# Performance work log

Hardware: AMD Instinct MI355X
Metric: run time of the kernel (lower is better)

Reference implementation:

```python
import jax, jax.numpy as jnp
import numpy as np

B, C, F = 4, 512, 2048
N, H = 8, 64  # header_size, header_channels
ALPHA = 1.0 / np.sqrt(H)


def setup_inputs() -> dict:
    key = jax.random.key(0)
    ks = jax.random.split(key, 6)
    return {
        "from_tensor": jax.random.normal(ks[0], (B, C, F), jnp.float32),
        "to_tensor": jax.random.normal(ks[1], (B, C, F), jnp.float32),
        "mask": jnp.ones((B, F, F), jnp.float32),
        "Wq": jax.random.normal(ks[2], (N * H, C), jnp.float32) * 0.02,
        "bq": jnp.zeros((N * H,), jnp.float32),
        "Wk": jax.random.normal(ks[3], (N * H, C), jnp.float32) * 0.02,
        "bk": jnp.zeros((N * H,), jnp.float32),
        "Wv": jax.random.normal(ks[4], (N * H, C), jnp.float32) * 0.02,
        "bv": jnp.zeros((N * H,), jnp.float32),
    }


def reference(from_tensor, to_tensor, mask, Wq, bq, Wk, bk, Wv, bv):
    b, _, f = from_tensor.shape
    t = to_tensor.shape[2]
    # Dense over channel dim: [B,C,F] -> [B,N*H,F], then split heads
    q = (jnp.einsum("oc,bcf->bof", Wq, from_tensor) + bq[None, :, None]).reshape(b, N, H, f)
    k = (jnp.einsum("oc,bct->bot", Wk, to_tensor) + bk[None, :, None]).reshape(b, N, H, t)
    v = (jnp.einsum("oc,bct->bot", Wv, to_tensor) + bv[None, :, None]).reshape(b, N, H, t)
    # score: q^T @ k -> [B,N,F,T]
    score = jnp.einsum("bnhf,bnht->bnft", q, k) * ALPHA
    score = score + (1.0 - mask[:, None]) * -100000.0
    probs = jax.nn.softmax(score, axis=-1)  # dropout=0 (inference)
    # context: probs @ v^T -> [B,N,F,H], transpose -> [B,N,H,F]
    ctx = jnp.einsum("bnft,bnht->bnhf", probs, v)
    return ctx.reshape(b, N * H, f)
```

## Files before the change

### kernel.cpp

```cpp
#include <hip/hip_runtime.h>

typedef __bf16 bf16x8 __attribute__((ext_vector_type(8)));
typedef float f32x4 __attribute__((ext_vector_type(4)));
typedef float f32x16 __attribute__((ext_vector_type(16)));
typedef unsigned short u16;
typedef u16 u16x8 __attribute__((ext_vector_type(8)));
typedef unsigned int u32;
typedef u32 u32x4 __attribute__((ext_vector_type(4)));
typedef unsigned long long u64;

#define DEVFN static __device__ __forceinline__

DEVFN u16 f2bf(float x) {
  u32 u = __builtin_bit_cast(u32, x);
  u32 r = u + 0x7FFFu + ((u >> 16) & 1u);
  return (u16)(r >> 16);
}

DEVFN float myexp2(float x) {
#if __has_builtin(__builtin_amdgcn_exp2f)
  return __builtin_amdgcn_exp2f(x);
#else
  return exp2f(x);
#endif
}

DEVFN u32 cvt_pk_bf16(float lo, float hi) {
  u32 r;
  asm("v_cvt_pk_bf16_f32 %0, %1, %2" : "=v"(r) : "v"(lo), "v"(hi));
  return r;
}

__global__ __launch_bounds__(512, 6) void proj_kernel(
    const float* __restrict__ from_t, const float* __restrict__ to_t,
    const float* __restrict__ Wq, const float* __restrict__ bq,
    const float* __restrict__ Wk, const float* __restrict__ bk,
    const float* __restrict__ Wv, const float* __restrict__ bv,
    u16* __restrict__ qt, u16* __restrict__ kt, u16* __restrict__ vt) {
  const int d     = blockIdx.x;
  const int xcd   = d & 7;
  const int b     = xcd >> 1;
  const int fh    = xcd & 1;
  const int local = d >> 3;
  const int mat   = local >> 5;
  const int o0    = ((local >> 3) & 3) * 128;
  const int f0    = (fh * 8 + (local & 7)) * 128;

  const float* X    = (mat == 0) ? from_t : to_t;
  const float* W    = (mat == 0) ? Wq : (mat == 1 ? Wk : Wv);
  const float* bias = (mat == 0) ? bq : (mat == 1 ? bk : bv);
  const bool isT = (mat < 2);

  __shared__ u16 Xs[128][64];
  __shared__ u16 Ws[128][64];

  const int tid  = threadIdx.x;
  const int lane = tid & 63;
  const int w    = tid >> 6;

  f32x4 acc[2][4];
#pragma unroll
  for (int i = 0; i < 2; ++i)
#pragma unroll
    for (int j = 0; j < 4; ++j)
#pragma unroll
      for (int r = 0; r < 4; ++r) acc[i][j][r] = 0.f;

  const int arow0 = (w & 3) * 32;
  const int brow0 = (w >> 2) * 64;

  for (int c0 = 0; c0 < 512; c0 += 64) {
    __syncthreads();
#pragma unroll
    for (int i = 0; i < 2; ++i) {
      const int task = tid + 512 * i;
      const int f = task & 127, cg = task >> 7;
      const float* xp = X + ((size_t)b * 512 + c0 + cg * 8) * 2048 + f0 + f;
      float xv[8];
#pragma unroll
      for (int j = 0; j < 8; ++j) xv[j] = xp[(size_t)j * 2048];
      u32x4 pk;
#pragma unroll
      for (int j = 0; j < 4; ++j) pk[j] = cvt_pk_bf16(xv[2 * j], xv[2 * j + 1]);
      *(u32x4*)&Xs[f][(cg ^ (f & 7)) * 8] = pk;
    }
#pragma unroll
    for (int i = 0; i < 2; ++i) {
      const int task = tid + 512 * i;
      const int o = task & 127, cg = task >> 7;
      const float* wp = W + (size_t)(o0 + o) * 512 + c0 + cg * 8;
      const float4 w0 = *(const float4*)(wp);
      const float4 w1 = *(const float4*)(wp + 4);
      u32x4 pk;
      pk[0] = cvt_pk_bf16(w0.x, w0.y);
      pk[1] = cvt_pk_bf16(w0.z, w0.w);
      pk[2] = cvt_pk_bf16(w1.x, w1.y);
      pk[3] = cvt_pk_bf16(w1.z, w1.w);
      *(u32x4*)&Ws[o][(cg ^ (o & 7)) * 8] = pk;
    }
    __syncthreads();

#pragma unroll
    for (int kk = 0; kk < 2; ++kk) {
      const int cb8 = kk * 4;
      bf16x8 afr[2], bfr[4];
#pragma unroll
      for (int mi = 0; mi < 2; ++mi) {
        const int row = arow0 + mi * 16 + (lane & 15);
        const int ch  = (cb8 + (lane >> 4)) ^ (row & 7);
        afr[mi] = *(const bf16x8*)&(isT ? Xs : Ws)[row][ch * 8];
      }
#pragma unroll
      for (int ni = 0; ni < 4; ++ni) {
        const int row = brow0 + ni * 16 + (lane & 15);
        const int ch  = (cb8 + (lane >> 4)) ^ (row & 7);
        bfr[ni] = *(const bf16x8*)&(isT ? Ws : Xs)[row][ch * 8];
      }
#pragma unroll
      for (int mi = 0; mi < 2; ++mi)
#pragma unroll
        for (int ni = 0; ni < 4; ++ni)
          acc[mi][ni] = __builtin_amdgcn_mfma_f32_16x16x32_bf16(
              afr[mi], bfr[ni], acc[mi][ni], 0, 0, 0);
    }
  }

  const float qscale = 0.18033688011112042f;
#pragma unroll
  for (int mi = 0; mi < 2; ++mi)
#pragma unroll
    for (int ni = 0; ni < 4; ++ni)
#pragma unroll
      for (int r = 0; r < 4; ++r) {
        const int rA = arow0 + mi * 16 + (lane >> 4) * 4 + r;
        const int cB = brow0 + ni * 16 + (lane & 15);
        int f, o;
        if (isT) { f = f0 + rA; o = o0 + cB; }
        else     { o = o0 + rA; f = f0 + cB; }
        float val = acc[mi][ni][r] + bias[o];
        if (mat == 0) val *= qscale;
        const u16 hv = f2bf(val);
        if (isT) {
          u16* dst = (mat == 0) ? qt : kt;
          dst[(((size_t)b * 8 + (o >> 6)) * 2048 + f) * 64 + (o & 63)] = hv;
        } else {
          vt[((size_t)b * 512 + o) * 2048 + f] = hv;
        }
      }
}

__global__ __launch_bounds__(256, 4) void maskflag_kernel(
    const float* __restrict__ mask, u32* __restrict__ fmask) {
  const int d    = blockIdx.x;
  const int b    = d >> 9;
  const int ft   = (d >> 5) & 15;
  const int tile = d & 31;
  const int t    = threadIdx.x;

  const float* base =
      mask + ((size_t)b * 2048 + ft * 128) * 2048 + tile * 64;
  bool ok = true;
#pragma unroll
  for (int i = 0; i < 8; ++i) {
    const int row = (t >> 4) * 8 + i;
    const float4 v = *(const float4*)(base + (size_t)row * 2048 + (t & 15) * 4);
    ok = ok && (v.x == 1.0f) && (v.y == 1.0f) && (v.z == 1.0f) && (v.w == 1.0f);
  }
  const u64 bal = __ballot(ok);
  __shared__ u32 wok[4];
  if ((t & 63) == 0) wok[t >> 6] = (bal == ~0ull) ? 1u : 0u;
  __syncthreads();
  if (t == 0) {
    const u32 allok = wok[0] & wok[1] & wok[2] & wok[3];
    if (allok) atomicOr(&fmask[b * 16 + ft], 1u << tile);
  }
}

#define SB __builtin_amdgcn_sched_barrier(0)

#define STAGE(BB, T0)                                                          \
  do {                                                                         \
    __builtin_amdgcn_global_load_lds(                                          \
        (const __attribute__((address_space(1))) void*)(ksrc1 + (size_t)(T0) * 64), \
        (__attribute__((address_space(3))) void*)&Ks[BB][w * 16][0], 16, 0, 0);\
    __builtin_amdgcn_global_load_lds(                                          \
        (const __attribute__((address_space(1))) void*)(ksrc2 + (size_t)(T0) * 64), \
        (__attribute__((address_space(3))) void*)&Ks[BB][w * 16 + 8][0], 16, 0, 0); \
    __builtin_amdgcn_global_load_lds(                                          \
        (const __attribute__((address_space(1))) void*)(vsrc1 + (T0)),         \
        (__attribute__((address_space(3))) void*)&Vs[BB][w * 16][0], 16, 0, 0);\
    __builtin_amdgcn_global_load_lds(                                          \
        (const __attribute__((address_space(1))) void*)(vsrc2 + (T0)),         \
        (__attribute__((address_space(3))) void*)&Vs[BB][w * 16 + 8][0], 16, 0, 0); \
  } while (0)

#define LDK(BUF)                                                               \
  do {                                                                         \
    _Pragma("unroll")                                                          \
    for (int kf_ = 0; kf_ < 4; ++kf_)                                          \
      _Pragma("unroll")                                                        \
      for (int mi_ = 0; mi_ < 2; ++mi_) {                                      \
        const int row_ = mi_ * 32 + fl;                                        \
        kreg[mi_][kf_] =                                                       \
            *(const bf16x8*)&Ks[BUF][row_][((kf_ * 2 + g) ^ (row_ & 7)) * 8];  \
      }                                                                        \
  } while (0)

#define LDV(BUF)                                                               \
  do {                                                                         \
    _Pragma("unroll")                                                          \
    for (int tf_ = 0; tf_ < 4; ++tf_)                                          \
      _Pragma("unroll")                                                        \
      for (int mh_ = 0; mh_ < 2; ++mh_) {                                      \
        const int row_ = mh_ * 32 + fl;                                        \
        vreg[mh_][tf_] =                                                       \
            *(const bf16x8*)&Vs[BUF][row_][((tf_ * 2 + g) ^ (row_ & 7)) * 8];  \
      }                                                                        \
  } while (0)

#define QKMM(SN)                                                               \
  do {                                                                         \
    _Pragma("unroll")                                                          \
    for (int m_ = 0; m_ < 2; ++m_)                                             \
      _Pragma("unroll")                                                        \
      for (int r_ = 0; r_ < 16; ++r_) SN[m_][r_] = 0.f;                        \
    _Pragma("unroll")                                                          \
    for (int kf_ = 0; kf_ < 4; ++kf_)                                          \
      _Pragma("unroll")                                                        \
      for (int mi_ = 0; mi_ < 2; ++mi_)                                        \
        SN[mi_] = __builtin_amdgcn_mfma_f32_32x32x16_bf16(kreg[mi_][kf_],      \
                                                          qf[kf_], SN[mi_],    \
                                                          0, 0, 0);            \
  } while (0)

#define ROUND(RB, SC, SN, T0)                                                  \
  {                                                                            \
    asm volatile("s_waitcnt vmcnt(0)" ::: "memory");                           \
    SB;                                                                        \
    __builtin_amdgcn_s_barrier();                                              \
    SB;                                                                        \
    LDV(RB);                                                                   \
    LDK((RB + 1) & 3);                                                         \
    SB;                                                                        \
    STAGE((RB + 2) & 3, ((T0) + 128) & 2047);                                  \
    SB;                                                                        \
    QKMM(SN);           \
                  \
    if (!((fmask >> ((T0) >> 6)) & 1u)) {                                      \
      float4 mk[8];                                                            \
      _Pragma("unroll")                                                        \
      for (int i_ = 0; i_ < 8; ++i_)                                           \
        mk[i_] = *(const float4*)(mrow + (T0) + (i_ >> 2) * 32 +               \
                                  (i_ & 3) * 8 + g * 4);                       \
      _Pragma("unroll")                                                        \
      for (int mi = 0; mi < 2; ++mi)                                           \
        _Pragma("unroll")                                                      \
        for (int q = 0; q < 4; ++q) {                                          \
          const float4 mv = mk[mi * 4 + q];                                    \
          SC[mi][q * 4 + 0] = fmaf(mv.x - 1.f, 144269.50408889634f, SC[mi][q * 4 + 0]); \
          SC[mi][q * 4 + 1] = fmaf(mv.y - 1.f, 144269.50408889634f, SC[mi][q * 4 + 1]); \
          SC[mi][q * 4 + 2] = fmaf(mv.z - 1.f, 144269.50408889634f, SC[mi][q * 4 + 2]); \
          SC[mi][q * 4 + 3] = fmaf(mv.w - 1.f, 144269.50408889634f, SC[mi][q * 4 + 3]); \
        }                                                                      \
    }                                                                          \
    float ps0 = 0.f, ps1 = 0.f, ps2 = 0.f, ps3 = 0.f;                          \
    _Pragma("unroll")                                                          \
    for (int mi = 0; mi < 2; ++mi)                                             \
      _Pragma("unroll")                                                        \
      for (int r = 0; r < 16; r += 4) {                                        \
        SC[mi][r + 0] = myexp2(SC[mi][r + 0]); ps0 += SC[mi][r + 0];           \
        SC[mi][r + 1] = myexp2(SC[mi][r + 1]); ps1 += SC[mi][r + 1];           \
        SC[mi][r + 2] = myexp2(SC[mi][r + 2]); ps2 += SC[mi][r + 2];           \
        SC[mi][r + 3] = myexp2(SC[mi][r + 3]); ps3 += SC[mi][r + 3];           \
      }                                                                        \
    {                                                                          \
      float ps = (ps0 + ps1) + (ps2 + ps3);                                    \
      ps += __shfl_xor(ps, 32, 64);                                            \
      L += ps;                                                                 \
    }                                                                          \
        \
    u32 dwv[2][4][2];                                                          \
    _Pragma("unroll")                                                          \
    for (int mi = 0; mi < 2; ++mi)                                             \
      _Pragma("unroll")                                                        \
      for (int q = 0; q < 4; ++q) {                                            \
        dwv[mi][q][0] = cvt_pk_bf16(SC[mi][q * 4 + 0], SC[mi][q * 4 + 1]);     \
        dwv[mi][q][1] = cvt_pk_bf16(SC[mi][q * 4 + 2], SC[mi][q * 4 + 3]);     \
      }                                                                        \
    _Pragma("unroll")                                                          \
    for (int tf = 0; tf < 4; ++tf) {                                           \
      const int m_ = tf >> 1, bq2 = tf & 1;                                    \
      u32 A0 = dwv[m_][bq2 * 2][0], A1 = dwv[m_][bq2 * 2][1];                  \
      u32 C0 = dwv[m_][bq2 * 2 + 1][0], C1 = dwv[m_][bq2 * 2 + 1][1];          \
      asm("v_permlane32_swap_b32 %0, %1" : "+v"(A0), "+v"(C0));                \
      asm("v_permlane32_swap_b32 %0, %1" : "+v"(A1), "+v"(C1));                \
      u32x4 pw; pw[0] = A0; pw[1] = A1; pw[2] = C0; pw[3] = C1;                \
      const bf16x8 pfr = __builtin_bit_cast(bf16x8, pw);                       \
      _Pragma("unroll")                                                        \
      for (int mih = 0; mih < 2; ++mih)                                        \
        ctx[mih] = __builtin_amdgcn_mfma_f32_32x32x16_bf16(vreg[mih][tf], pfr, \
                                                           ctx[mih], 0, 0, 0); \
    }                                                                          \
  }

__global__ __launch_bounds__(256, 2) void attn_kernel(
    const float* __restrict__ mask, const u32* __restrict__ fmaskbuf,
    const u16* __restrict__ qt, const u16* __restrict__ kt,
    const u16* __restrict__ vt, float* __restrict__ out) {
  const int d     = blockIdx.x;
  const int xcd   = d & 7;
  const int b     = xcd >> 1;
  const int fthi  = xcd & 1;
  const int local = d >> 3;
  const int n     = local & 7;
  const int ft    = fthi * 8 + (local >> 3);

  const int tid  = threadIdx.x;
  const int lane = tid & 63;
  const int w    = tid >> 6;
  const int g    = lane >> 5;
  const int fl   = lane & 31;
  const int f    = ft * 128 + w * 32 + fl;

  const u16* qtb = qt + ((size_t)b * 8 + n) * 2048 * 64;
  const u16* ktb = kt + ((size_t)b * 8 + n) * 2048 * 64;
  const u16* vb  = vt + ((size_t)b * 512 + n * 64) * 2048;
  const float* mrow = mask + ((size_t)b * 2048 + f) * 2048;
  const u32 fmask = fmaskbuf ? fmaskbuf[b * 16 + ft] : 0u;

  __shared__ u16 Ks[4][64][64];
  __shared__ u16 Vs[4][64][64];

  bf16x8 qf[4];
#pragma unroll
  for (int kf = 0; kf < 4; ++kf)
    qf[kf] = *(const bf16x8*)(qtb + (size_t)f * 64 + kf * 16 + g * 8);

  f32x16 ctx[2];
#pragma unroll
  for (int m = 0; m < 2; ++m)
#pragma unroll
    for (int r = 0; r < 16; ++r) ctx[m][r] = 0.f;
  float L = 0.f;

  const int sr1 = w * 16 + (lane >> 3), sr2 = sr1 + 8;
  const int sc1 = (lane & 7) ^ (sr1 & 7), sc2 = (lane & 7) ^ (sr2 & 7);
  const u16* ksrc1 = ktb + (size_t)sr1 * 64 + sc1 * 8;
  const u16* ksrc2 = ktb + (size_t)sr2 * 64 + sc2 * 8;
  const u16* vsrc1 = vb + (size_t)sr1 * 2048 + sc1 * 8;
  const u16* vsrc2 = vb + (size_t)sr2 * 2048 + sc2 * 8;

  bf16x8 kreg[2][4], vreg[2][4];
  f32x16 sA[2], sB[2];

  STAGE(0, 0);
  STAGE(1, 64);
  SB;
  asm volatile("s_waitcnt vmcnt(0)" ::: "memory");
  SB;
  __builtin_amdgcn_s_barrier();
  SB;
  LDK(0);
  QKMM(sA);

  for (int t0 = 0; t0 < 2048; t0 += 256) {
    ROUND(0, sA, sB, t0);
    ROUND(1, sB, sA, t0 + 64);
    ROUND(2, sA, sB, t0 + 128);
    ROUND(3, sB, sA, t0 + 192);
  }

  const float Linv = 1.0f / L;
#pragma unroll
  for (int mih = 0; mih < 2; ++mih)
#pragma unroll
    for (int r = 0; r < 16; ++r) {
      const int h = mih * 32 + (r & 3) + 8 * (r >> 2) + 4 * g;
      out[((size_t)b * 512 + n * 64 + h) * 2048 + f] = ctx[mih][r] * Linv;
    }
}

extern "C" void kernel_launch(void* const* d_in, const int* in_sizes, int n_in,
                              void* d_out, int out_size, void* d_ws, size_t ws_size,
                              hipStream_t stream) {
  const float* from_t = (const float*)d_in[0];
  const float* to_t   = (const float*)d_in[1];
  const float* mask   = (const float*)d_in[2];
  const float* Wq     = (const float*)d_in[3];
  const float* bq     = (const float*)d_in[4];
  const float* Wk     = (const float*)d_in[5];
  const float* bk     = (const float*)d_in[6];
  const float* Wv     = (const float*)d_in[7];
  const float* bv     = (const float*)d_in[8];
  float* out = (float*)d_out;

  u16* qt = (u16*)d_ws;
  u16* kt = qt + (size_t)4 * 8 * 2048 * 64;
  u16* vt = kt + (size_t)4 * 8 * 2048 * 64;
  const size_t base = (size_t)24 * 1024 * 1024;
  u32* fl = (ws_size >= base + 256) ? (u32*)((char*)d_ws + base) : nullptr;

  proj_kernel<<<dim3(768), 512, 0, stream>>>(from_t, to_t, Wq, bq, Wk, bk,
                                             Wv, bv, qt, kt, vt);
  if (fl) {
    hipMemsetAsync(fl, 0, 64 * sizeof(u32), stream);
    maskflag_kernel<<<dim3(2048), 256, 0, stream>>>(mask, fl);
  }
  attn_kernel<<<dim3(512), 256, 0, stream>>>(mask, fl, qt, kt, vt, out);
}
```

Measured before the change: 112.9 us.

## Fuse mask-flag scan into projection kernel as extra interleaved blocks

Merges the separate mask-scanning kernel into the projection kernel by adding 1024 extra blocks that scan mask tiles alongside the 768 projection blocks, saving one kernel launch. The bandwidth-bound mask reads can then overlap with the compute-bound projection GEMM. Mask loads now use nontemporal hints and each block covers a 128x128 tile, setting two flag bits. This adds grid index arithmetic, and because the projection and scan blocks share one kernel, the scan blocks run under the projection kernel's 512-thread launch configuration.

```diff
diff --git a/kernel.cpp b/kernel.cpp
--- a/kernel.cpp
+++ b/kernel.cpp
@@ -3,6 +3,7 @@
 typedef __bf16 bf16x8 __attribute__((ext_vector_type(8)));
 typedef float f32x4 __attribute__((ext_vector_type(4)));
 typedef float f32x16 __attribute__((ext_vector_type(16)));
+typedef float fvec4 __attribute__((ext_vector_type(4)));
 typedef unsigned short u16;
 typedef u16 u16x8 __attribute__((ext_vector_type(8)));
 typedef unsigned int u32;
@@ -31,17 +32,64 @@
   return r;
 }
 
-__global__ __launch_bounds__(512, 6) void proj_kernel(
+__global__ __launch_bounds__(512, 6) void projflag_kernel(
     const float* __restrict__ from_t, const float* __restrict__ to_t,
+    const float* __restrict__ mask,
     const float* __restrict__ Wq, const float* __restrict__ bq,
     const float* __restrict__ Wk, const float* __restrict__ bk,
     const float* __restrict__ Wv, const float* __restrict__ bv,
-    u16* __restrict__ qt, u16* __restrict__ kt, u16* __restrict__ vt) {
-  const int d     = blockIdx.x;
-  const int xcd   = d & 7;
+    u16* __restrict__ qt, u16* __restrict__ kt, u16* __restrict__ vt,
+    u32* __restrict__ fmask) {
+  __shared__ u16 Xs[128][64];
+  __shared__ u16 Ws[128][64];
+
+  const int bid = blockIdx.x;
+  const int xcd = bid & 7;
+  const int li  = bid >> 3;
+  const int grp = li / 7, rem = li % 7;
+  const int tid = threadIdx.x;
+
+  if (rem >= 3) {
+    if (!fmask) return;
+    const int idx = xcd * 128 + grp * 4 + (rem - 3);
+    const int b   = idx >> 8;
+    const int ft  = (idx >> 4) & 15;
+    const int tp  = idx & 15;
+    const int r   = tid >> 2;
+    const int q   = tid & 3;
+    const float* base = mask + ((size_t)(b * 2048 + ft * 128 + r)) * 2048 +
+                        tp * 128 + q * 32;
+    bool ok = true;
+#pragma unroll
+    for (int j = 0; j < 8; ++j) {
+      const fvec4 v = __builtin_nontemporal_load((const fvec4*)(base) + j);
+      ok = ok && (v[0] == 1.0f) && (v[1] == 1.0f) && (v[2] == 1.0f) &&
+           (v[3] == 1.0f);
+    }
+    const bool lo = (q < 2);
+    const u64 blo = __ballot(ok || !lo);
+    const u64 bhi = __ballot(ok || lo);
+    u32* wok = (u32*)&Xs[0][0];
+    const int w8 = tid >> 6;
+    if ((tid & 63) == 0) {
+      wok[w8]     = (blo == ~0ull) ? 1u : 0u;
+      wok[8 + w8] = (bhi == ~0ull) ? 1u : 0u;
+    }
+    __syncthreads();
+    if (tid == 0) {
+      u32 alo = 1u, ahi = 1u;
+#pragma unroll
+      for (int i = 0; i < 8; ++i) { alo &= wok[i]; ahi &= wok[8 + i]; }
+      const u32 bits = (alo ? (1u << (2 * tp)) : 0u) |
+                       (ahi ? (1u << (2 * tp + 1)) : 0u);
+      if (bits) atomicOr(&fmask[b * 16 + ft], bits);
+    }
+    return;
+  }
+
   const int b     = xcd >> 1;
   const int fh    = xcd & 1;
-  const int local = d >> 3;
+  const int local = grp * 3 + rem;
   const int mat   = local >> 5;
   const int o0    = ((local >> 3) & 3) * 128;
   const int f0    = (fh * 8 + (local & 7)) * 128;
@@ -51,10 +99,6 @@
   const float* bias = (mat == 0) ? bq : (mat == 1 ? bk : bv);
   const bool isT = (mat < 2);
 
-  __shared__ u16 Xs[128][64];
-  __shared__ u16 Ws[128][64];
-
-  const int tid  = threadIdx.x;
   const int lane = tid & 63;
   const int w    = tid >> 6;
 
@@ -149,33 +193,6 @@
       }
 }
 
-__global__ __launch_bounds__(256, 4) void maskflag_kernel(
-    const float* __restrict__ mask, u32* __restrict__ fmask) {
-  const int d    = blockIdx.x;
-  const int b    = d >> 9;
-  const int ft   = (d >> 5) & 15;
-  const int tile = d & 31;
-  const int t    = threadIdx.x;
-
-  const float* base =
-      mask + ((size_t)b * 2048 + ft * 128) * 2048 + tile * 64;
-  bool ok = true;
-#pragma unroll
-  for (int i = 0; i < 8; ++i) {
-    const int row = (t >> 4) * 8 + i;
-    const float4 v = *(const float4*)(base + (size_t)row * 2048 + (t & 15) * 4);
-    ok = ok && (v.x == 1.0f) && (v.y == 1.0f) && (v.z == 1.0f) && (v.w == 1.0f);
-  }
-  const u64 bal = __ballot(ok);
-  __shared__ u32 wok[4];
-  if ((t & 63) == 0) wok[t >> 6] = (bal == ~0ull) ? 1u : 0u;
-  __syncthreads();
-  if (t == 0) {
-    const u32 allok = wok[0] & wok[1] & wok[2] & wok[3];
-    if (allok) atomicOr(&fmask[b * 16 + ft], 1u << tile);
-  }
-}
-
 #define SB __builtin_amdgcn_sched_barrier(0)
 
 #define STAGE(BB, T0)                                                          \
@@ -400,11 +417,8 @@
   const size_t base = (size_t)24 * 1024 * 1024;
   u32* fl = (ws_size >= base + 256) ? (u32*)((char*)d_ws + base) : nullptr;
 
-  proj_kernel<<<dim3(768), 512, 0, stream>>>(from_t, to_t, Wq, bq, Wk, bk,
-                                             Wv, bv, qt, kt, vt);
-  if (fl) {
-    hipMemsetAsync(fl, 0, 64 * sizeof(u32), stream);
-    maskflag_kernel<<<dim3(2048), 256, 0, stream>>>(mask, fl);
-  }
+  if (fl) (void)hipMemsetAsync(fl, 0, 64 * sizeof(u32), stream);
+  projflag_kernel<<<dim3(1792), 512, 0, stream>>>(
+      from_t, to_t, mask, Wq, bq, Wk, bk, Wv, bv, qt, kt, vt, fl);
   attn_kernel<<<dim3(512), 256, 0, stream>>>(mask, fl, qt, kt, vt, out);
 }
```

Result: slower. 137.1 us (+21.5%).
